# Performance work log

Measured on AMD Instinct MI355X. Metric: run time of the kernel, lower is better.

The kernel has to match this reference:

```python
import jax, jax.numpy as jnp
import numpy as np

N_LOWER, N_UPPER, Q_LOWER, Q_UPPER = 128, 128, 64, 64

def setup_inputs() -> dict:
    key = jax.random.key(0)
    ks = jax.random.split(key, 6)
    P = jax.random.uniform(ks[0], (64, N_LOWER, Q_LOWER), dtype=jnp.float32)
    weight = 0.1 * jax.random.normal(ks[1], (N_UPPER, N_LOWER), dtype=jnp.float32)
    bias_abs = 0.1 * jax.random.normal(ks[2], (N_UPPER, 1), dtype=jnp.float32)
    bias_q = 0.1 * jax.random.normal(ks[3], (N_UPPER, 1), dtype=jnp.float32)
    lambda_abs = 0.1 * jax.random.normal(ks[4], (N_UPPER, 1), dtype=jnp.float32)
    lambda_q = 0.1 * jax.random.normal(ks[5], (N_UPPER, 1), dtype=jnp.float32)
    return {"P": P, "weight": weight, "bias_abs": bias_abs, "bias_q": bias_q,
            "lambda_abs": lambda_abs, "lambda_q": lambda_q}

def reference(P, weight, bias_abs, bias_q, lambda_abs, lambda_q):
    # base distance kernel: D[l, m] = exp(-(m/q_lower - l/q_upper)^2)
    lower = jnp.arange(Q_LOWER, dtype=jnp.float32) / Q_LOWER          # [q_lower]
    upper = jnp.arange(Q_UPPER, dtype=jnp.float32) / Q_UPPER          # [q_upper]
    logD = -(lower[None, :] - upper[:, None]) ** 2                    # [q_upper, q_lower] = log(D)
    # T[j,k,l,m] = D[l,m] ** weight[j,k] = exp(weight[j,k] * logD[l,m])
    T = jnp.exp(weight[:, :, None, None] * logD[None, None, :, :])    # [n_up, n_low, q_up, q_low]
    # Pw[i,j,k,l] = sum_m T[j,k,l,m] * P[i,k,m]   (batched small mat-vec)
    Pw = jnp.einsum('jklm,ikm->ijkl', T, P)                           # [b, n_up, n_low, q_up]
    Pw = jnp.clip(Pw, 1e-15, 1e15)
    logsum = jnp.sum(jnp.log(Pw), axis=2)                             # [b, n_up, q_up]
    # log-domain bias: -b_q*(s0/q - lam_q)^2 - b_a*|s0/q - lam_a|
    s = jnp.arange(Q_UPPER, dtype=jnp.float32)[None, :] / Q_UPPER     # [1, q_up]
    B = -bias_q * (s - lambda_q) ** 2 - bias_abs * jnp.abs(s - lambda_abs)  # [n_up, q_up]
    return jax.nn.softmax(logsum + B[None, :, :], axis=2)             # [b, n_up, q_up]
```

## Files before the change

kernel.cpp:

```cpp
#include <hip/hip_runtime.h>
#include <hip/hip_fp16.h>


typedef _Float16 half8 __attribute__((ext_vector_type(8)));
typedef float float4v __attribute__((ext_vector_type(4)));

__global__ __launch_bounds__(256)
void drn_pack(const float* __restrict__ P, _Float16* __restrict__ pf16) {
    const int tid = blockIdx.x * 256 + threadIdx.x;
    const int ln = tid & 63;
    const int ks = (tid >> 6) & 1;
    const int it = (tid >> 7) & 3;
    const int k  = tid >> 9;
    const int i  = it * 16 + (ln & 15);
    const int m0 = ks * 32 + (ln >> 4) * 8;
    const float* src = P + ((size_t)i * 128 + k) * 64 + m0;
    half8 h;
#pragma unroll
    for (int t = 0; t < 8; ++t) h[t] = (_Float16)src[t];
    ((uint4*)pf16)[tid] = __builtin_bit_cast(uint4, h);
}

__global__ __launch_bounds__(256, 2)
void drn_main(const _Float16* __restrict__ pf16,
              const float* __restrict__ weight,
              float* __restrict__ part) {
    __shared__ _Float16 tab[4][1024];
    __shared__ float red[2][4096];

    const int tid  = threadIdx.x;
    const int lane = tid & 63;
    const int wv   = tid >> 6;
    const int j    = blockIdx.x >> 2;
    const int g    = blockIdx.x & 3;

    const int la   = lane & 15;
    const int quad = lane >> 4;
    const int r    = (63 - la) & 7;
    const int kbase = g * 32 + wv * 8;
    _Float16* mytab = tab[wv];

    float prod[16][4];
#pragma unroll
    for (int t = 0; t < 16; ++t)
#pragma unroll
        for (int q = 0; q < 4; ++q) prod[t][q] = 1.0f;

    const float4v z4 = {0.f, 0.f, 0.f, 0.f};
    const uint4* bbase = (const uint4*)pf16;

    uint4 Bc[8], Bn[8];
#pragma unroll
    for (int f = 0; f < 8; ++f)
        Bc[f] = bbase[(kbase * 8 + f) * 64 + lane];

    for (int kk = 0; kk < 8; ++kk) {
        const int k = kbase + kk;
        const float a = weight[j * 128 + k] * (1.0f / 4096.0f);

        const float d0 = 63.0f - (float)lane;
        const float d1 = (float)lane + 1.0f;
        const _Float16 h0 = (_Float16)__expf(-a * d0 * d0);
        const _Float16 h1 = (_Float16)__expf(-a * d1 * d1);
        __builtin_amdgcn_wave_barrier();
#pragma unroll
        for (int rr = 0; rr < 8; ++rr) {
            if (lane >= rr) mytab[rr * 128 + lane - rr] = h0;
            mytab[rr * 128 + lane + 64 - rr] = h1;
        }
        __builtin_amdgcn_wave_barrier();

        uint4 A[8];
#pragma unroll
        for (int lt = 0; lt < 4; ++lt)
#pragma unroll
            for (int ks = 0; ks < 2; ++ks) {
                const int eb = 63 - (lt * 16 + la) + ks * 32 + quad * 8;
                A[lt * 2 + ks] = *(const uint4*)&mytab[r * 128 + (eb - r)];
            }
        __builtin_amdgcn_wave_barrier();

        if (kk < 7) {
#pragma unroll
            for (int f = 0; f < 8; ++f)
                Bn[f] = bbase[((k + 1) * 8 + f) * 64 + lane];
        }

#pragma unroll
        for (int lt = 0; lt < 4; ++lt) {
#pragma unroll
            for (int it = 0; it < 4; ++it) {
                float4v acc = __builtin_amdgcn_mfma_f32_16x16x32_f16(
                    __builtin_bit_cast(half8, A[lt * 2 + 0]),
                    __builtin_bit_cast(half8, Bc[it * 2 + 0]), z4, 0, 0, 0);
                acc = __builtin_amdgcn_mfma_f32_16x16x32_f16(
                    __builtin_bit_cast(half8, A[lt * 2 + 1]),
                    __builtin_bit_cast(half8, Bc[it * 2 + 1]), acc, 0, 0, 0);
#pragma unroll
                for (int q = 0; q < 4; ++q) prod[lt * 4 + it][q] *= acc[q];
            }
        }
        if (kk < 7) {
#pragma unroll
            for (int f = 0; f < 8; ++f) Bc[f] = Bn[f];
        }
    }

    float lg[16][4];
#pragma unroll
    for (int t = 0; t < 16; ++t)
#pragma unroll
        for (int q = 0; q < 4; ++q) lg[t][q] = __logf(prod[t][q]);

    if (wv < 2) {
#pragma unroll
        for (int lt = 0; lt < 4; ++lt)
#pragma unroll
            for (int it = 0; it < 4; ++it)
#pragma unroll
                for (int q = 0; q < 4; ++q)
                    red[wv][(lt * 16 + quad * 4 + q) * 64 + it * 16 + la] = lg[lt * 4 + it][q];
    }
    __syncthreads();
    if (wv >= 2) {
#pragma unroll
        for (int lt = 0; lt < 4; ++lt)
#pragma unroll
            for (int it = 0; it < 4; ++it)
#pragma unroll
                for (int q = 0; q < 4; ++q)
                    red[wv - 2][(lt * 16 + quad * 4 + q) * 64 + it * 16 + la] += lg[lt * 4 + it][q];
    }
    __syncthreads();

    float* dst = part + ((size_t)(j * 4 + g) * 64) * 64;
#pragma unroll
    for (int n = 0; n < 16; ++n) {
        const int e = tid * 16 + n;
        const float v = red[0][e] + red[1][e];
        const int l = e >> 6, i = e & 63;
        dst[i * 64 + l] = v;
    }
}

__global__ __launch_bounds__(256)
void drn_softmax(const float* __restrict__ part,
                 const float* __restrict__ bias_abs,
                 const float* __restrict__ bias_q,
                 const float* __restrict__ lambda_abs,
                 const float* __restrict__ lambda_q,
                 float* __restrict__ out) {
    const int tid = threadIdx.x;
    const int l   = tid & 63;
    const int wv  = tid >> 6;
    const int pair = blockIdx.x * 4 + wv;
    const int i = pair >> 7;
    const int j = pair & 127;

    const float* pp = part + ((size_t)(j * 4) * 64 + i) * 64 + l;
    float v = pp[0] + pp[4096] + pp[2 * 4096] + pp[3 * 4096];

    const float s  = (float)l * (1.0f / 64.0f);
    const float dq = s - lambda_q[j];
    v += -bias_q[j] * dq * dq - bias_abs[j] * fabsf(s - lambda_abs[j]);

    float mx = v;
#pragma unroll
    for (int off = 32; off > 0; off >>= 1)
        mx = fmaxf(mx, __shfl_xor(mx, off, 64));
    const float e = __expf(v - mx);
    float sm = e;
#pragma unroll
    for (int off = 32; off > 0; off >>= 1)
        sm += __shfl_xor(sm, off, 64);

    out[((size_t)i * 128 + j) * 64 + l] = e / sm;
}

extern "C" void kernel_launch(void* const* d_in, const int* in_sizes, int n_in,
                              void* d_out, int out_size, void* d_ws, size_t ws_size,
                              hipStream_t stream) {
    const float* P          = (const float*)d_in[0];
    const float* weight     = (const float*)d_in[1];
    const float* bias_abs   = (const float*)d_in[2];
    const float* bias_q     = (const float*)d_in[3];
    const float* lambda_abs = (const float*)d_in[4];
    const float* lambda_q   = (const float*)d_in[5];
    float* outp = (float*)d_out;

    _Float16* pf16 = (_Float16*)d_ws;
    float* part    = (float*)((char*)d_ws + (1 << 20));

    drn_pack<<<dim3(256), dim3(256), 0, stream>>>(P, pf16);
    drn_main<<<dim3(512), dim3(256), 0, stream>>>(pf16, weight, part);
    drn_softmax<<<dim3(2048), dim3(256), 0, stream>>>(
        part, bias_abs, bias_q, lambda_abs, lambda_q, outp);
}
```

Baseline: 85.06 us.

## Fuse main product kernel with softmax and double-buffer the LDS exp table

Merges the log-product kernel and the softmax kernel into one launch. Each block now owns a full j row across all 128 k (8 waves of 16 k each) and half of the batch, so the partial log-sums never go to global memory. The exp table is double-buffered so the next k's table is written while the current one is read. Products are flushed to log every 8 steps to avoid underflow over 16 multiplications. This removes one launch and the partial buffer round-trip, but grid parallelism drops from 512 to 256 blocks and the per-block reduction now passes through LDS.

After: 82.60 us, median of 2. 2.9% less time.

```diff
diff --git a/kernel.cpp b/kernel.cpp
--- a/kernel.cpp
+++ b/kernel.cpp
@@ -1,5 +1,4 @@
 #include <hip/hip_runtime.h>
-#include <hip/hip_fp16.h>
 
 
 typedef _Float16 half8 __attribute__((ext_vector_type(8)));
@@ -21,75 +20,97 @@
     ((uint4*)pf16)[tid] = __builtin_bit_cast(uint4, h);
 }
 
-__global__ __launch_bounds__(256, 2)
-void drn_main(const _Float16* __restrict__ pf16,
-              const float* __restrict__ weight,
-              float* __restrict__ part) {
-    __shared__ _Float16 tab[4][1024];
-    __shared__ float red[2][4096];
-
-    const int tid  = threadIdx.x;
-    const int lane = tid & 63;
-    const int wv   = tid >> 6;
-    const int j    = blockIdx.x >> 2;
-    const int g    = blockIdx.x & 3;
-
-    const int la   = lane & 15;
-    const int quad = lane >> 4;
-    const int r    = (63 - la) & 7;
-    const int kbase = g * 32 + wv * 8;
-    _Float16* mytab = tab[wv];
-
-    float prod[16][4];
-#pragma unroll
-    for (int t = 0; t < 16; ++t)
-#pragma unroll
-        for (int q = 0; q < 4; ++q) prod[t][q] = 1.0f;
+__global__ __launch_bounds__(512, 2)
+void drn_fused(const _Float16* __restrict__ pf16,
+               const float* __restrict__ weight,
+               const float* __restrict__ bias_abs,
+               const float* __restrict__ bias_q,
+               const float* __restrict__ lambda_abs,
+               const float* __restrict__ lambda_q,
+               float* __restrict__ out) {
+    __shared__ _Float16 tab[8][2][1024];
+    __shared__ float red[4][64][36];
+
+    const int tid   = threadIdx.x;
+    const int lane  = tid & 63;
+    const int wv    = tid >> 6;
+    const int j     = blockIdx.x >> 1;
+    const int ihalf = blockIdx.x & 1;
+
+    const int la    = lane & 15;
+    const int quad  = lane >> 4;
+    const int rrep  = (63 - la) & 7;
+    const int kbase = wv * 16;
+
+    float wk[16];
+#pragma unroll
+    for (int kk = 0; kk < 16; ++kk) wk[kk] = weight[j * 128 + kbase + kk];
+
+    float prod[8][4], logacc[8][4];
+#pragma unroll
+    for (int t = 0; t < 8; ++t)
+#pragma unroll
+        for (int q = 0; q < 4; ++q) { prod[t][q] = 1.0f; logacc[t][q] = 0.0f; }
 
     const float4v z4 = {0.f, 0.f, 0.f, 0.f};
-    const uint4* bbase = (const uint4*)pf16;
-
-    uint4 Bc[8], Bn[8];
-#pragma unroll
-    for (int f = 0; f < 8; ++f)
-        Bc[f] = bbase[(kbase * 8 + f) * 64 + lane];
-
-    for (int kk = 0; kk < 8; ++kk) {
-        const int k = kbase + kk;
-        const float a = weight[j * 128 + k] * (1.0f / 4096.0f);
-
-        const float d0 = 63.0f - (float)lane;
-        const float d1 = (float)lane + 1.0f;
+    const uint4* bb = (const uint4*)pf16;
+    const int boff = ihalf * 4;
+
+    uint4 Bc[4], Bn[4];
+#pragma unroll
+    for (int f = 0; f < 4; ++f)
+        Bc[f] = bb[(kbase * 8 + boff + f) * 64 + lane];
+
+    const float d0 = 63.0f - (float)lane;
+    const float d1 = (float)lane + 1.0f;
+
+    {
+        const float a = wk[0] * (1.0f / 4096.0f);
         const _Float16 h0 = (_Float16)__expf(-a * d0 * d0);
         const _Float16 h1 = (_Float16)__expf(-a * d1 * d1);
-        __builtin_amdgcn_wave_barrier();
+        _Float16* dst = tab[wv][0];
 #pragma unroll
         for (int rr = 0; rr < 8; ++rr) {
-            if (lane >= rr) mytab[rr * 128 + lane - rr] = h0;
-            mytab[rr * 128 + lane + 64 - rr] = h1;
-        }
-        __builtin_amdgcn_wave_barrier();
-
+            if (lane >= rr) dst[rr * 128 + lane - rr] = h0;
+            dst[rr * 128 + lane + 64 - rr] = h1;
+        }
+    }
+    __builtin_amdgcn_wave_barrier();
+
+    for (int kk = 0; kk < 16; ++kk) {
+        const _Float16* cur = tab[wv][kk & 1];
         uint4 A[8];
 #pragma unroll
         for (int lt = 0; lt < 4; ++lt)
 #pragma unroll
             for (int ks = 0; ks < 2; ++ks) {
                 const int eb = 63 - (lt * 16 + la) + ks * 32 + quad * 8;
-                A[lt * 2 + ks] = *(const uint4*)&mytab[r * 128 + (eb - r)];
+                A[lt * 2 + ks] = *(const uint4*)&cur[rrep * 128 + (eb - rrep)];
             }
+
+        if (kk < 15) {
+            const float a = wk[kk + 1] * (1.0f / 4096.0f);
+            const _Float16 h0 = (_Float16)__expf(-a * d0 * d0);
+            const _Float16 h1 = (_Float16)__expf(-a * d1 * d1);
+            _Float16* dst = tab[wv][(kk + 1) & 1];
+#pragma unroll
+            for (int rr = 0; rr < 8; ++rr) {
+                if (lane >= rr) dst[rr * 128 + lane - rr] = h0;
+                dst[rr * 128 + lane + 64 - rr] = h1;
+            }
+        }
         __builtin_amdgcn_wave_barrier();
 
-        if (kk < 7) {
-#pragma unroll
-            for (int f = 0; f < 8; ++f)
-                Bn[f] = bbase[((k + 1) * 8 + f) * 64 + lane];
-        }
-
-#pragma unroll
-        for (int lt = 0; lt < 4; ++lt) {
-#pragma unroll
-            for (int it = 0; it < 4; ++it) {
+        if (kk < 15) {
+#pragma unroll
+            for (int f = 0; f < 4; ++f)
+                Bn[f] = bb[((kbase + kk + 1) * 8 + boff + f) * 64 + lane];
+        }
+
+#pragma unroll
+        for (int lt = 0; lt < 4; ++lt)
+#pragma unroll
+            for (int it = 0; it < 2; ++it) {
                 float4v acc = __builtin_amdgcn_mfma_f32_16x16x32_f16(
                     __builtin_bit_cast(half8, A[lt * 2 + 0]),
                     __builtin_bit_cast(half8, Bc[it * 2 + 0]), z4, 0, 0, 0);
@@ -97,84 +118,73 @@
                     __builtin_bit_cast(half8, A[lt * 2 + 1]),
                     __builtin_bit_cast(half8, Bc[it * 2 + 1]), acc, 0, 0, 0);
 #pragma unroll
-                for (int q = 0; q < 4; ++q) prod[lt * 4 + it][q] *= acc[q];
+                for (int q = 0; q < 4; ++q) prod[lt * 2 + it][q] *= acc[q];
             }
-        }
-        if (kk < 7) {
-#pragma unroll
-            for (int f = 0; f < 8; ++f) Bc[f] = Bn[f];
-        }
-    }
-
-    float lg[16][4];
-#pragma unroll
-    for (int t = 0; t < 16; ++t)
-#pragma unroll
-        for (int q = 0; q < 4; ++q) lg[t][q] = __logf(prod[t][q]);
-
-    if (wv < 2) {
-#pragma unroll
-        for (int lt = 0; lt < 4; ++lt)
-#pragma unroll
-            for (int it = 0; it < 4; ++it)
+
+        if (kk == 7) {
+#pragma unroll
+            for (int t = 0; t < 8; ++t)
+#pragma unroll
+                for (int q = 0; q < 4; ++q) {
+                    logacc[t][q] += __logf(prod[t][q]);
+                    prod[t][q] = 1.0f;
+                }
+        }
+        if (kk < 15) {
+#pragma unroll
+            for (int f = 0; f < 4; ++f) Bc[f] = Bn[f];
+        }
+    }
+#pragma unroll
+    for (int t = 0; t < 8; ++t)
+#pragma unroll
+        for (int q = 0; q < 4; ++q) logacc[t][q] += __logf(prod[t][q]);
+
+    if (wv < 4) {
+#pragma unroll
+        for (int lt = 0; lt < 4; ++lt)
+#pragma unroll
+            for (int it = 0; it < 2; ++it)
 #pragma unroll
                 for (int q = 0; q < 4; ++q)
-                    red[wv][(lt * 16 + quad * 4 + q) * 64 + it * 16 + la] = lg[lt * 4 + it][q];
+                    red[wv][lt * 16 + quad * 4 + q][it * 16 + la] = logacc[lt * 2 + it][q];
     }
     __syncthreads();
-    if (wv >= 2) {
-#pragma unroll
-        for (int lt = 0; lt < 4; ++lt)
-#pragma unroll
-            for (int it = 0; it < 4; ++it)
+    if (wv >= 4) {
+#pragma unroll
+        for (int lt = 0; lt < 4; ++lt)
+#pragma unroll
+            for (int it = 0; it < 2; ++it)
 #pragma unroll
                 for (int q = 0; q < 4; ++q)
-                    red[wv - 2][(lt * 16 + quad * 4 + q) * 64 + it * 16 + la] += lg[lt * 4 + it][q];
+                    red[wv - 4][lt * 16 + quad * 4 + q][it * 16 + la] += logacc[lt * 2 + it][q];
     }
     __syncthreads();
 
-    float* dst = part + ((size_t)(j * 4 + g) * 64) * 64;
-#pragma unroll
-    for (int n = 0; n < 16; ++n) {
-        const int e = tid * 16 + n;
-        const float v = red[0][e] + red[1][e];
-        const int l = e >> 6, i = e & 63;
-        dst[i * 64 + l] = v;
-    }
-}
-
-__global__ __launch_bounds__(256)
-void drn_softmax(const float* __restrict__ part,
-                 const float* __restrict__ bias_abs,
-                 const float* __restrict__ bias_q,
-                 const float* __restrict__ lambda_abs,
-                 const float* __restrict__ lambda_q,
-                 float* __restrict__ out) {
-    const int tid = threadIdx.x;
-    const int l   = tid & 63;
-    const int wv  = tid >> 6;
-    const int pair = blockIdx.x * 4 + wv;
-    const int i = pair >> 7;
-    const int j = pair & 127;
-
-    const float* pp = part + ((size_t)(j * 4) * 64 + i) * 64 + l;
-    float v = pp[0] + pp[4096] + pp[2 * 4096] + pp[3 * 4096];
-
-    const float s  = (float)l * (1.0f / 64.0f);
-    const float dq = s - lambda_q[j];
-    v += -bias_q[j] * dq * dq - bias_abs[j] * fabsf(s - lambda_abs[j]);
-
-    float mx = v;
-#pragma unroll
-    for (int off = 32; off > 0; off >>= 1)
-        mx = fmaxf(mx, __shfl_xor(mx, off, 64));
-    const float e = __expf(v - mx);
-    float sm = e;
-#pragma unroll
-    for (int off = 32; off > 0; off >>= 1)
-        sm += __shfl_xor(sm, off, 64);
-
-    out[((size_t)i * 128 + j) * 64 + l] = e / sm;
+    const float bq = bias_q[j],   lq = lambda_q[j];
+    const float ba = bias_abs[j], la2 = lambda_abs[j];
+    const float s  = (float)lane * (1.0f / 64.0f);
+    const float dq = s - lq;
+    const float Bjl = -bq * dq * dq - ba * fabsf(s - la2);
+
+#pragma unroll
+    for (int r = 0; r < 4; ++r) {
+        const int il = wv * 4 + r;
+        float v = red[0][lane][il] + red[1][lane][il]
+                + red[2][lane][il] + red[3][lane][il] + Bjl;
+
+        float mx = v;
+#pragma unroll
+        for (int off = 32; off > 0; off >>= 1)
+            mx = fmaxf(mx, __shfl_xor(mx, off, 64));
+        const float e = __expf(v - mx);
+        float sm = e;
+#pragma unroll
+        for (int off = 32; off > 0; off >>= 1)
+            sm += __shfl_xor(sm, off, 64);
+
+        out[((size_t)(ihalf * 32 + il) * 128 + j) * 64 + lane] = e / sm;
+    }
 }
 
 extern "C" void kernel_launch(void* const* d_in, const int* in_sizes, int n_in,
@@ -189,10 +199,8 @@
     float* outp = (float*)d_out;
 
     _Float16* pf16 = (_Float16*)d_ws;
-    float* part    = (float*)((char*)d_ws + (1 << 20));
 
     drn_pack<<<dim3(256), dim3(256), 0, stream>>>(P, pf16);
-    drn_main<<<dim3(512), dim3(256), 0, stream>>>(pf16, weight, part);
-    drn_softmax<<<dim3(2048), dim3(256), 0, stream>>>(
-        part, bias_abs, bias_q, lambda_abs, lambda_q, outp);
+    drn_fused<<<dim3(256), dim3(512), 0, stream>>>(
+        pf16, weight, bias_abs, bias_q, lambda_abs, lambda_q, outp);
 }
```
